# Kernel tuning notes

Measured on AMD Instinct MI355X. Metric: run time of the kernel, lower is better.

## Reference

```python
import jax, jax.numpy as jnp
import numpy as np

B, N, D, A = 2048, 32, 64, 8
MAX_ACTION = 1.0
VARIANCE = 1.0


def setup_inputs() -> dict:
    key = jax.random.key(0)
    k1, k2, k3, k4, k5 = jax.random.split(key, 5)
    mean = jax.random.normal(k1, (B, D), dtype=jnp.float32)
    # SPD covariance: small-scale L L^T + 0.1 I
    L = jax.random.normal(k2, (B, D, D), dtype=jnp.float32) * 0.05
    covariance = jnp.einsum('bij,bkj->bik', L, L) + 0.1 * jnp.eye(D, dtype=jnp.float32)
    centers = jax.random.normal(k3, (N, D), dtype=jnp.float32) * 0.5
    weights = jax.random.normal(k4, (N, A), dtype=jnp.float32) * 0.1
    lengthscales = jnp.ones((D,), dtype=jnp.float32) + 0.1 * jax.random.uniform(k5, (D,), dtype=jnp.float32)
    return {"mean": mean, "covariance": covariance, "centers": centers,
            "weights": weights, "lengthscales": lengthscales}


def squash_sin(mean, covariance, max_action):
    # mean: (B, K); covariance: (B, K, K)
    K = mean.shape[-1]
    ma = jnp.full((K,), max_action, dtype=mean.dtype)
    diag_cov = jnp.diagonal(covariance, axis1=-2, axis2=-1)          # (B, K)
    squashed_mean = ma * jnp.exp(-diag_cov / 2.0) * jnp.sin(mean)
    lq = -(diag_cov[..., :, None] + diag_cov[..., None, :]) / 2.0
    q = jnp.exp(lq)
    mean_diff = mean[..., :, None] - mean[..., None, :]
    mean_sum = mean[..., :, None] + mean[..., None, :]
    sq_cov = ((jnp.exp(lq + covariance) - q) * jnp.cos(mean_diff)
              - (jnp.exp(lq - covariance) - q) * jnp.cos(mean_sum))
    outer_max = ma[None, :] * ma[:, None]
    sq_cov = outer_max * sq_cov / 2.0
    # diag_embed of (B, K) -> (B, K, K)
    cross = (ma * jnp.exp(-diag_cov / 2.0) * jnp.cos(mean))[..., :, None] * jnp.eye(K, dtype=mean.dtype)
    return squashed_mean, sq_cov, cross


def reference(mean, covariance, centers, weights, lengthscales):
    b = mean.shape[0]
    inv_l = 1.0 / lengthscales                                        # (D,)
    # B_mat = diag(inv_l) @ cov @ diag(inv_l) + I  (B, D, D)
    B_mat = covariance * (inv_l[:, None] * inv_l[None, :]) + jnp.eye(D, dtype=mean.dtype)
    inp = centers[None, :, :] - mean[:, None, :]                      # (B, N, D)
    scaled_inp = inp * inv_l                                          # (B, N, D)
    t = jnp.swapaxes(jnp.linalg.solve(B_mat, jnp.swapaxes(scaled_inp, -1, -2)), -1, -2)  # (B, N, D)
    exp_term = jnp.exp(-0.5 * jnp.sum(scaled_inp * t, axis=-1))       # (B, N)
    _, log_det = jnp.linalg.slogdet(B_mat)                            # (B,)
    normalizer = VARIANCE * jnp.exp(-0.5 * log_det)
    phi_mean = normalizer[:, None] * exp_term                         # (B, N)
    action_mean = phi_mean @ weights                                  # (B, A)

    t_scaled = t * inv_l                                              # (B, N, D)
    cross_cov = jnp.einsum('bnd,bna->bda', t_scaled, phi_mean[..., None] * weights)  # (B, D, A)

    diff = centers[:, None, :] - centers[None, :, :]                  # (N, N, D)
    center_bar = (centers[:, None, :] + centers[None, :, :]) / 2.0    # (N, N, D)
    inv_lambda = 1.0 / lengthscales ** 2
    exp1 = -0.25 * jnp.sum(diff ** 2 * inv_lambda, axis=-1)           # (N, N)
    B_q = covariance + jnp.diag(lengthscales ** 2 / 2.0)[None]        # (B, D, D)
    z = center_bar[None] - mean[:, None, None, :]                     # (B, N, N, D)
    z_flat = z.reshape(b, N * N, D)
    solved = jnp.swapaxes(jnp.linalg.solve(B_q, jnp.swapaxes(z_flat, -1, -2)), -1, -2)
    exp2 = (-0.5 * jnp.sum(z_flat * solved, axis=-1)).reshape(b, N, N)
    log_det_lh = jnp.sum(jnp.log(lengthscales ** 2 / 2.0))
    _, log_det_bq = jnp.linalg.slogdet(B_q)
    c_q = jnp.exp(0.5 * (log_det_lh - log_det_bq))                    # (B,)
    Q = (VARIANCE ** 2) * c_q[:, None, None] * jnp.exp(exp1[None] + exp2)  # (B, N, N)

    action_cov = jnp.einsum('na,bnm,mc->bac', weights, Q, weights)    # (B, A, A)
    action_cov = action_cov - action_mean[:, :, None] * action_mean[:, None, :]
    action_cov = (action_cov + jnp.swapaxes(action_cov, -1, -2)) / 2.0
    action_cov = action_cov + jnp.eye(A, dtype=mean.dtype) * 1e-6

    action_mean, action_cov, C = squash_sin(action_mean, action_cov, MAX_ACTION)
    cross_cov = jnp.einsum('bda,bac->bdc', cross_cov, C)
    return (action_mean, action_cov, cross_cov)
```

## Files before the change

kernel.cpp:

```cpp
#include <hip/hip_runtime.h>
#include <math.h>


#define DD 64
#define NN 32
#define AA 8
#define NBATCH 2048
#define STR 68
#define W9 9

__device__ __forceinline__ float frl(float v, int lane) {
    return __int_as_float(__builtin_amdgcn_readlane(__float_as_int(v), lane));
}

__global__ void rbf_prep(const float* __restrict__ centers,
                         const float* __restrict__ ls,
                         float* __restrict__ ws) {
    __shared__ float cen_s[NN * DD];
    __shared__ float il2_s[DD];
    int t = threadIdx.x;
    for (int e = t; e < NN * DD; e += 256) cen_s[e] = centers[e];
    if (t < DD) { float l = ls[t]; il2_s[t] = 1.0f / (l * l); }
    __syncthreads();
    int p = blockIdx.x * 256 + t;
    if (p < NN * NN) {
        int n = p >> 5, m = p & 31;
        float acc = 0.f;
        for (int d = 0; d < DD; ++d) {
            float df = cen_s[n * DD + d] - cen_s[m * DD + d];
            acc += df * df * il2_s[d];
        }
        ws[p] = -0.25f * acc;
    }
    if (blockIdx.x == 0 && t < DD) {
        float l = ls[t];
        float v = logf(0.5f * l * l);
        #pragma unroll
        for (int o = 1; o < 64; o <<= 1) v += __shfl_xor(v, o, 64);
        if (t == 0) ws[NN * NN] = v;
    }
}

__device__ __forceinline__ void factor_panel(float (&A)[4][4], const int p,
    float* __restrict__ LmT, float* __restrict__ diag_s, float* __restrict__ invd_s,
    const int lw)
{
    const int rb  = lw & 15;
    const int cbl = lw >> 4;
    const int c0  = 16 * p + 4 * cbl;
    const int r0  = 4 * rb;
    #pragma unroll
    for (int jj = 0; jj < 16; ++jj) {
        const int q  = jj >> 2;
        const int ci = jj & 3;
        const int j  = 16 * p + jj;
        const int fsrc = rb | (q << 4);
        const int hsrc = (4 * p + cbl) | (q << 4);
        const int dsrc = (4 * p + q) | (q << 4);
        float d  = frl(A[ci][ci], dsrc);
        float f0 = __shfl(A[0][ci], fsrc, 64);
        float f1 = __shfl(A[1][ci], fsrc, 64);
        float f2 = __shfl(A[2][ci], fsrc, 64);
        float f3 = __shfl(A[3][ci], fsrc, 64);
        float h0 = __shfl(A[0][ci], hsrc, 64);
        float h1 = __shfl(A[1][ci], hsrc, 64);
        float h2 = __shfl(A[2][ci], hsrc, 64);
        float h3 = __shfl(A[3][ci], hsrc, 64);
        float id = __builtin_amdgcn_rcpf(d);
        float fr[4];
        fr[0] = (r0 + 0 > j) ? f0 : 0.f;
        fr[1] = (r0 + 1 > j) ? f1 : 0.f;
        fr[2] = (r0 + 2 > j) ? f2 : 0.f;
        fr[3] = (r0 + 3 > j) ? f3 : 0.f;
        float hc[4];
        hc[0] = (c0 + 0 > j) ? h0 * id : 0.f;
        hc[1] = (c0 + 1 > j) ? h1 * id : 0.f;
        hc[2] = (c0 + 2 > j) ? h2 * id : 0.f;
        hc[3] = (c0 + 3 > j) ? h3 * id : 0.f;
        #pragma unroll
        for (int s = 0; s < 4; ++s)
            #pragma unroll
            for (int c = 0; c < 4; ++c)
                A[s][c] -= fr[s] * hc[c];
        if (cbl == 0) {
            float4 v = make_float4(fr[0] * id, fr[1] * id, fr[2] * id, fr[3] * id);
            *(float4*)&LmT[j * STR + r0] = v;
        }
        if (lw == jj) { diag_s[j] = d; invd_s[j] = id; }
    }
}

__device__ __forceinline__ void trailing_one(float (&A)[4][4], const int p,
    const float* __restrict__ LmT, const float* __restrict__ diag_s,
    const int rb, const int cbX)
{
    #pragma unroll 2
    for (int kk = 0; kk < 16; ++kk) {
        const int k = 16 * p + kk;
        const float4 Lr = *(const float4*)&LmT[k * STR + 4 * rb];
        const float4 Lc = *(const float4*)&LmT[k * STR + 4 * cbX];
        const float dk = diag_s[k];
        const float h0 = Lc.x * dk, h1 = Lc.y * dk, h2 = Lc.z * dk, h3 = Lc.w * dk;
        A[0][0] -= Lr.x * h0; A[0][1] -= Lr.x * h1; A[0][2] -= Lr.x * h2; A[0][3] -= Lr.x * h3;
        A[1][0] -= Lr.y * h0; A[1][1] -= Lr.y * h1; A[1][2] -= Lr.y * h2; A[1][3] -= Lr.y * h3;
        A[2][0] -= Lr.z * h0; A[2][1] -= Lr.z * h1; A[2][2] -= Lr.z * h2; A[2][3] -= Lr.z * h3;
        A[3][0] -= Lr.w * h0; A[3][1] -= Lr.w * h1; A[3][2] -= Lr.w * h2; A[3][3] -= Lr.w * h3;
    }
}

__global__ __launch_bounds__(256, 3) void rbf_main(
    const float* __restrict__ mean,
    const float* __restrict__ cov,
    const float* __restrict__ centers,
    const float* __restrict__ weights,
    const float* __restrict__ ls,
    const float* __restrict__ ws,
    float* __restrict__ out)
{
    __shared__ __align__(16) float LmT1[DD * STR];
    __shared__ __align__(16) float U2s[DD * STR];
    __shared__ __align__(16) float phiwc[NN * AA];
    __shared__ float diag1[DD], invd1[DD], diag2[DD], invd2[DD];
    __shared__ float mean_s[DD], invl_s[DD], l2h_s[DD];
    __shared__ float w9_s[NN * W9], U_s[NN * W9];
    __shared__ float am_s[AA], acr_s[AA * W9], Ca_s[AA];
    __shared__ float ldlh_s;

    float* const LmT2 = U2s;
    float* const H_s  = U2s;
    float* const x_s  = U2s + NN * STR;
    float* const cp_s = U2s + NN * STR;

    const int t   = threadIdx.x;
    const int b   = blockIdx.x;
    const int lw  = t & 63;
    const int wv  = t >> 6;
    const int rb  = t & 15;
    const int cb  = t >> 4;
    const int cb1 = (cb + 8) & 15;
    const int wp1 = (wv + 2) & 3;
    const int l8  = t & 7;
    const float* cvb = cov + (size_t)b * DD * DD;

    if (t < DD) {
        float l = ls[t];
        invl_s[t] = 1.0f / l;
        l2h_s[t]  = 0.5f * l * l;
        mean_s[t] = mean[(size_t)b * DD + t];
    }
    w9_s[(t >> 3) * W9 + (t & 7)] = weights[t];
    if (t == 0) ldlh_s = ws[NN * NN];
    __syncthreads();

    float A1[4][4], A2[4][4];
    {
        #pragma unroll
        for (int c = 0; c < 4; ++c) {
            const int gr = 4 * cb + c;
            const float4 cv = *(const float4*)(cvb + (size_t)gr * DD + 4 * rb);
            A2[0][c] = cv.x + ((4*rb+0 == gr) ? l2h_s[gr] : 0.0f);
            A2[1][c] = cv.y + ((4*rb+1 == gr) ? l2h_s[gr] : 0.0f);
            A2[2][c] = cv.z + ((4*rb+2 == gr) ? l2h_s[gr] : 0.0f);
            A2[3][c] = cv.w + ((4*rb+3 == gr) ? l2h_s[gr] : 0.0f);
        }
        const float il0 = invl_s[4*rb+0], il1 = invl_s[4*rb+1],
                    il2 = invl_s[4*rb+2], il3 = invl_s[4*rb+3];
        #pragma unroll
        for (int c = 0; c < 4; ++c) {
            const int gr = 4 * cb1 + c;
            const float4 cv = *(const float4*)(cvb + (size_t)gr * DD + 4 * rb);
            const float ilc = invl_s[gr];
            A1[0][c] = cv.x * il0 * ilc + ((4*rb+0 == gr) ? 1.0f : 0.0f);
            A1[1][c] = cv.y * il1 * ilc + ((4*rb+1 == gr) ? 1.0f : 0.0f);
            A1[2][c] = cv.z * il2 * ilc + ((4*rb+2 == gr) ? 1.0f : 0.0f);
            A1[3][c] = cv.w * il3 * ilc + ((4*rb+3 == gr) ? 1.0f : 0.0f);
        }
    }

    if (wv == 0) factor_panel(A2, 0, LmT2, diag2, invd2, lw);
    if (wv == 2) factor_panel(A1, 0, LmT1, diag1, invd1, lw);
    #pragma unroll 1
    for (int p = 0; p < 3; ++p) {
        __syncthreads();
        if (wv  >= p + 1) trailing_one(A2, p, LmT2, diag2, rb, cb);
        if (wp1 >= p + 1) trailing_one(A1, p, LmT1, diag1, rb, cb1);
        if (wv == p + 1)         factor_panel(A2, p + 1, LmT2, diag2, invd2, lw);
        if (wv == ((p + 3) & 3)) factor_panel(A1, p + 1, LmT1, diag1, invd1, lw);
    }
    __syncthreads();

    float logdet1, cq;
    {
        float v1 = logf(diag1[lw]);
        float v2 = logf(diag2[lw]);
        #pragma unroll
        for (int o = 1; o < 64; o <<= 1) {
            v1 += __shfl_xor(v1, o, 64);
            v2 += __shfl_xor(v2, o, 64);
        }
        logdet1 = v1;
        cq = expf(0.5f * (ldlh_s - v2));
    }

    const int gr8 = lw >> 3;
    float xs0[8], xs1[8], xs2[8], xs3[8];
    if (wv == 0) {
        #pragma unroll
        for (int rr = 0; rr < 4; ++rr) {
            const int n = gr8 + 8 * rr;
            const float4 ca = *(const float4*)(centers + n * DD + 8 * l8);
            const float4 cz = *(const float4*)(centers + n * DD + 8 * l8 + 4);
            float da[8] = {ca.x,ca.y,ca.z,ca.w,cz.x,cz.y,cz.z,cz.w};
            float* xp = (rr == 0) ? xs0 : (rr == 1) ? xs1 : (rr == 2) ? xs2 : xs3;
            #pragma unroll
            for (int s = 0; s < 8; ++s) {
                const int i = 8 * l8 + s;
                xp[s] = (da[s] - mean_s[i]) * invl_s[i];
            }
        }
        for (int k8 = 0; k8 < 8; ++k8) {
            #pragma unroll
            for (int kk = 0; kk < 8; ++kk) {
                const int k = 8 * k8 + kk;
                const int src = (lw & 56) | k8;
                float z0 = __shfl(xs0[kk], src, 64);
                float z1 = __shfl(xs1[kk], src, 64);
                float z2 = __shfl(xs2[kk], src, 64);
                float z3 = __shfl(xs3[kk], src, 64);
                const float4 LA = *(const float4*)&LmT1[k * STR + 8 * l8];
                const float4 LB = *(const float4*)&LmT1[k * STR + 8 * l8 + 4];
                float l1[8] = {LA.x,LA.y,LA.z,LA.w,LB.x,LB.y,LB.z,LB.w};
                #pragma unroll
                for (int s = 0; s < 8; ++s) {
                    xs0[s] -= l1[s] * z0;
                    xs1[s] -= l1[s] * z1;
                    xs2[s] -= l1[s] * z2;
                    xs3[s] -= l1[s] * z3;
                }
            }
        }
        #pragma unroll
        for (int rr = 0; rr < 4; ++rr) {
            const int n = gr8 + 8 * rr;
            const float* xp = (rr == 0) ? xs0 : (rr == 1) ? xs1 : (rr == 2) ? xs2 : xs3;
            float qf = 0.f;
            #pragma unroll
            for (int s = 0; s < 8; ++s) qf += xp[s] * xp[s] * invd1[8 * l8 + s];
            qf += __shfl_xor(qf, 1, 64);
            qf += __shfl_xor(qf, 2, 64);
            qf += __shfl_xor(qf, 4, 64);
            float ph = expf(-0.5f * (logdet1 + qf));
            phiwc[n * AA + l8] = ph * w9_s[n * W9 + l8];
        }
    } else if (wv == 1) {
        float x0[8], x1v[8], x2v[8], x3v[8];
        #pragma unroll
        for (int rr = 0; rr < 4; ++rr) {
            const int n = gr8 + 8 * rr;
            const float4 ca = *(const float4*)(centers + n * DD + 8 * l8);
            const float4 cz = *(const float4*)(centers + n * DD + 8 * l8 + 4);
            float da[8] = {ca.x,ca.y,ca.z,ca.w,cz.x,cz.y,cz.z,cz.w};
            float* xp = (rr == 0) ? x0 : (rr == 1) ? x1v : (rr == 2) ? x2v : x3v;
            #pragma unroll
            for (int s = 0; s < 8; ++s) {
                const int i = 8 * l8 + s;
                xp[s] = 0.5f * (da[s] - mean_s[i]);
            }
        }
        for (int k8 = 0; k8 < 8; ++k8) {
            #pragma unroll
            for (int kk = 0; kk < 8; ++kk) {
                const int k = 8 * k8 + kk;
                const int src = (lw & 56) | k8;
                float z0 = __shfl(x0[kk],  src, 64);
                float z1 = __shfl(x1v[kk], src, 64);
                float z2 = __shfl(x2v[kk], src, 64);
                float z3 = __shfl(x3v[kk], src, 64);
                const float4 MA = *(const float4*)&LmT2[k * STR + 8 * l8];
                const float4 MB = *(const float4*)&LmT2[k * STR + 8 * l8 + 4];
                float l2[8] = {MA.x,MA.y,MA.z,MA.w,MB.x,MB.y,MB.z,MB.w};
                #pragma unroll
                for (int s = 0; s < 8; ++s) {
                    x0[s]  -= l2[s] * z0;
                    x1v[s] -= l2[s] * z1;
                    x2v[s] -= l2[s] * z2;
                    x3v[s] -= l2[s] * z3;
                }
            }
        }
        #pragma unroll
        for (int rr = 0; rr < 4; ++rr) {
            const int n = gr8 + 8 * rr;
            const float* xp = (rr == 0) ? x0 : (rr == 1) ? x1v : (rr == 2) ? x2v : x3v;
            float h[8];
            #pragma unroll
            for (int s = 0; s < 8; ++s) h[s] = xp[s] * sqrtf(invd2[8 * l8 + s]);
            *(float4*)&H_s[n * STR + 8 * l8]     = make_float4(h[0],h[1],h[2],h[3]);
            *(float4*)&H_s[n * STR + 8 * l8 + 4] = make_float4(h[4],h[5],h[6],h[7]);
        }
    }
    __syncthreads();

    if (wv == 0) {
        #pragma unroll
        for (int rr = 0; rr < 4; ++rr) {
            const int n = gr8 + 8 * rr;
            const float* xp = (rr == 0) ? xs0 : (rr == 1) ? xs1 : (rr == 2) ? xs2 : xs3;
            *(float4*)&x_s[n * STR + 8 * l8]     = make_float4(xp[0],xp[1],xp[2],xp[3]);
            *(float4*)&x_s[n * STR + 8 * l8 + 4] = make_float4(xp[4],xp[5],xp[6],xp[7]);
        }
        const int aa = lw >> 3;
        float y[8] = {0.f,0.f,0.f,0.f,0.f,0.f,0.f,0.f};
        for (int n = 0; n < NN; ++n) {
            const float pw = phiwc[n * AA + aa];
            const float4 xa = *(const float4*)&x_s[n * STR + 8 * l8];
            const float4 xb = *(const float4*)&x_s[n * STR + 8 * l8 + 4];
            y[0] += xa.x * pw; y[1] += xa.y * pw;
            y[2] += xa.z * pw; y[3] += xa.w * pw;
            y[4] += xb.x * pw; y[5] += xb.y * pw;
            y[6] += xb.z * pw; y[7] += xb.w * pw;
        }
        #pragma unroll
        for (int s = 0; s < 8; ++s) y[s] *= invd1[8 * l8 + s];
        for (int i8 = 7; i8 >= 0; --i8) {
            #pragma unroll
            for (int ii = 7; ii >= 0; --ii) {
                const int i = 8 * i8 + ii;
                const float4 r0 = *(const float4*)&LmT1[i * STR + 8 * l8];
                const float4 r1 = *(const float4*)&LmT1[i * STR + 8 * l8 + 4];
                float part = r0.x*y[0] + r0.y*y[1] + r0.z*y[2] + r0.w*y[3]
                           + r1.x*y[4] + r1.y*y[5] + r1.z*y[6] + r1.w*y[7];
                part += __shfl_xor(part, 1, 64);
                part += __shfl_xor(part, 2, 64);
                part += __shfl_xor(part, 4, 64);
                if (l8 == i8) y[ii] -= part;
            }
        }
        #pragma unroll
        for (int s = 0; s < 8; ++s)
            cp_s[(8 * l8 + s) * W9 + aa] = y[s] * invl_s[8 * l8 + s];
    } else if (wv == 3) {
        if (lw < AA) {
            const int a = lw;
            float am = 0.f;
            for (int n = 0; n < NN; ++n) am += phiwc[n * AA + a];
            am_s[a] = am;
        }
    } else {
        const int g16 = (lw >> 3) + 8 * (wv - 1);
        const int n0 = g16, n1 = g16 + 16;
        float acc0[4] = {0.f,0.f,0.f,0.f}, acc1[4] = {0.f,0.f,0.f,0.f};
        const int rot = 2 * l8;
        #pragma unroll 2
        for (int e = 0; e < 16; ++e) {
            const int e4 = 4 * ((e + rot) & 15);
            const float4 hn0 = *(const float4*)&H_s[n0 * STR + e4];
            const float4 hn1 = *(const float4*)&H_s[n1 * STR + e4];
            #pragma unroll
            for (int mm = 0; mm < 4; ++mm) {
                const float4 hm = *(const float4*)&H_s[(4 * l8 + mm) * STR + e4];
                {
                    float s0 = hn0.x + hm.x, s1 = hn0.y + hm.y;
                    float s2 = hn0.z + hm.z, s3 = hn0.w + hm.w;
                    acc0[mm] += s0*s0 + s1*s1 + s2*s2 + s3*s3;
                }
                {
                    float s0 = hn1.x + hm.x, s1 = hn1.y + hm.y;
                    float s2 = hn1.z + hm.z, s3 = hn1.w + hm.w;
                    acc1[mm] += s0*s0 + s1*s1 + s2*s2 + s3*s3;
                }
            }
        }
        const float4 e1a = *(const float4*)&ws[n0 * NN + 4 * l8];
        const float4 e1b = *(const float4*)&ws[n1 * NN + 4 * l8];
        float Q0a = cq * expf(e1a.x - 0.5f * acc0[0]);
        float Q1a = cq * expf(e1a.y - 0.5f * acc0[1]);
        float Q2a = cq * expf(e1a.z - 0.5f * acc0[2]);
        float Q3a = cq * expf(e1a.w - 0.5f * acc0[3]);
        float Q0b = cq * expf(e1b.x - 0.5f * acc1[0]);
        float Q1b = cq * expf(e1b.y - 0.5f * acc1[1]);
        float Q2b = cq * expf(e1b.z - 0.5f * acc1[2]);
        float Q3b = cq * expf(e1b.w - 0.5f * acc1[3]);
        float ua[8], ub[8];
        #pragma unroll
        for (int a = 0; a < 8; ++a) {
            const float w0 = w9_s[(4*l8+0)*W9 + a], w1 = w9_s[(4*l8+1)*W9 + a];
            const float w2 = w9_s[(4*l8+2)*W9 + a], w3 = w9_s[(4*l8+3)*W9 + a];
            ua[a] = Q0a*w0 + Q1a*w1 + Q2a*w2 + Q3a*w3;
            ub[a] = Q0b*w0 + Q1b*w1 + Q2b*w2 + Q3b*w3;
            ua[a] += __shfl_xor(ua[a], 1, 64);
            ua[a] += __shfl_xor(ua[a], 2, 64);
            ua[a] += __shfl_xor(ua[a], 4, 64);
            ub[a] += __shfl_xor(ub[a], 1, 64);
            ub[a] += __shfl_xor(ub[a], 2, 64);
            ub[a] += __shfl_xor(ub[a], 4, 64);
        }
        float uva = (l8 == 0) ? ua[0] : (l8 == 1) ? ua[1] : (l8 == 2) ? ua[2] : (l8 == 3) ? ua[3]
                  : (l8 == 4) ? ua[4] : (l8 == 5) ? ua[5] : (l8 == 6) ? ua[6] : ua[7];
        float uvb = (l8 == 0) ? ub[0] : (l8 == 1) ? ub[1] : (l8 == 2) ? ub[2] : (l8 == 3) ? ub[3]
                  : (l8 == 4) ? ub[4] : (l8 == 5) ? ub[5] : (l8 == 6) ? ub[6] : ub[7];
        U_s[n0 * W9 + l8] = uva;
        U_s[n1 * W9 + l8] = uvb;
    }
    __syncthreads();

    if (t < 64) {
        const int a = t >> 3, c = t & 7;
        float acc2 = 0.f;
        for (int n = 0; n < NN; ++n) acc2 += w9_s[n * W9 + a] * U_s[n * W9 + c];
        acr_s[a * W9 + c] = acc2;
    }
    __syncthreads();

    float* out0 = out;
    float* out1 = out + (size_t)NBATCH * AA;
    float* out2 = out + (size_t)NBATCH * AA + (size_t)NBATCH * AA * AA;
    if (t < 64) {
        const int a = t >> 3, c = t & 7;
        const float ama = am_s[a], amc = am_s[c];
        const float vac = 0.5f * (acr_s[a * W9 + c] + acr_s[c * W9 + a])
                        - ama * amc + ((a == c) ? 1e-6f : 0.0f);
        const float dca = acr_s[a * W9 + a] - ama * ama + 1e-6f;
        const float dcc = acr_s[c * W9 + c] - amc * amc + 1e-6f;
        const float q = expf(-0.5f * (dca + dcc));
        const float sq = 0.5f * q * (expm1f(vac) * cosf(ama - amc)
                                   - expm1f(-vac) * cosf(ama + amc));
        out1[(size_t)b * 64 + t] = sq;
        if (t < AA) {
            float dct = acr_s[t * W9 + t] - am_s[t] * am_s[t] + 1e-6f;
            float e = expf(-0.5f * dct);
            out0[(size_t)b * AA + t] = e * sinf(am_s[t]);
            Ca_s[t] = e * cosf(am_s[t]);
        }
    }
    __syncthreads();
    #pragma unroll
    for (int e = 0; e < 2; ++e) {
        int idx = t + 256 * e;
        out2[(size_t)b * 512 + idx] = cp_s[(idx >> 3) * W9 + (idx & 7)] * Ca_s[idx & 7];
    }
}

extern "C" void kernel_launch(void* const* d_in, const int* in_sizes, int n_in,
                              void* d_out, int out_size, void* d_ws, size_t ws_size,
                              hipStream_t stream) {
    (void)in_sizes; (void)n_in; (void)out_size; (void)ws_size;
    const float* mean    = (const float*)d_in[0];
    const float* cov     = (const float*)d_in[1];
    const float* centers = (const float*)d_in[2];
    const float* weights = (const float*)d_in[3];
    const float* ls      = (const float*)d_in[4];
    float* ws = (float*)d_ws;
    float* o  = (float*)d_out;
    rbf_prep<<<4, 256, 0, stream>>>(centers, ls, ws);
    rbf_main<<<NBATCH, 256, 0, stream>>>(mean, cov, centers, weights, ls, ws, o);
}
```

Before: 199.5 us.

## XOR-swizzle LmT shared layout and block the backward triangular solve

Stores the LDL factor rows in shared memory with an XOR swizzle over 8-wide column groups, and updates the Cholesky trailing loop and the forward solves to read through the same swizzle. This is meant to cut LDS bank conflicts. The backward substitution becomes a blocked 8x8 scheme: the diagonal block's values are broadcast by shuffle, solved redundantly in registers, and then the earlier blocks are updated. That replaces the three-step shuffle reduction per row. The swizzle has to stay consistent across every reader of LmT, or results will be wrong.

Measured after the change: 199.4 us. Within noise of the previous version (-0.0%).

```diff
diff --git a/kernel.cpp b/kernel.cpp
--- a/kernel.cpp
+++ b/kernel.cpp
@@ -83,8 +83,9 @@
             for (int c = 0; c < 4; ++c)
                 A[s][c] -= fr[s] * hc[c];
         if (cbl == 0) {
+            const int wo = 8 * ((rb >> 1) ^ ((j >> 3) & 7)) + 4 * (rb & 1);
             float4 v = make_float4(fr[0] * id, fr[1] * id, fr[2] * id, fr[3] * id);
-            *(float4*)&LmT[j * STR + r0] = v;
+            *(float4*)&LmT[j * STR + wo] = v;
         }
         if (lw == jj) { diag_s[j] = d; invd_s[j] = id; }
     }
@@ -97,8 +98,9 @@
     #pragma unroll 2
     for (int kk = 0; kk < 16; ++kk) {
         const int k = 16 * p + kk;
-        const float4 Lr = *(const float4*)&LmT[k * STR + 4 * rb];
-        const float4 Lc = *(const float4*)&LmT[k * STR + 4 * cbX];
+        const int cs = (k >> 3) & 7;
+        const float4 Lr = *(const float4*)&LmT[k * STR + 8*((rb >>1)^cs) + 4*(rb &1)];
+        const float4 Lc = *(const float4*)&LmT[k * STR + 8*((cbX>>1)^cs) + 4*(cbX&1)];
         const float dk = diag_s[k];
         const float h0 = Lc.x * dk, h1 = Lc.y * dk, h2 = Lc.z * dk, h3 = Lc.w * dk;
         A[0][0] -= Lr.x * h0; A[0][1] -= Lr.x * h1; A[0][2] -= Lr.x * h2; A[0][3] -= Lr.x * h3;
@@ -219,6 +221,7 @@
             }
         }
         for (int k8 = 0; k8 < 8; ++k8) {
+            const int kg = 8 * (l8 ^ k8);
             #pragma unroll
             for (int kk = 0; kk < 8; ++kk) {
                 const int k = 8 * k8 + kk;
@@ -227,8 +230,8 @@
                 float z1 = __shfl(xs1[kk], src, 64);
                 float z2 = __shfl(xs2[kk], src, 64);
                 float z3 = __shfl(xs3[kk], src, 64);
-                const float4 LA = *(const float4*)&LmT1[k * STR + 8 * l8];
-                const float4 LB = *(const float4*)&LmT1[k * STR + 8 * l8 + 4];
+                const float4 LA = *(const float4*)&LmT1[k * STR + kg];
+                const float4 LB = *(const float4*)&LmT1[k * STR + kg + 4];
                 float l1[8] = {LA.x,LA.y,LA.z,LA.w,LB.x,LB.y,LB.z,LB.w};
                 #pragma unroll
                 for (int s = 0; s < 8; ++s) {
@@ -268,6 +271,7 @@
             }
         }
         for (int k8 = 0; k8 < 8; ++k8) {
+            const int kg = 8 * (l8 ^ k8);
             #pragma unroll
             for (int kk = 0; kk < 8; ++kk) {
                 const int k = 8 * k8 + kk;
@@ -276,8 +280,8 @@
                 float z1 = __shfl(x1v[kk], src, 64);
                 float z2 = __shfl(x2v[kk], src, 64);
                 float z3 = __shfl(x3v[kk], src, 64);
-                const float4 MA = *(const float4*)&LmT2[k * STR + 8 * l8];
-                const float4 MB = *(const float4*)&LmT2[k * STR + 8 * l8 + 4];
+                const float4 MA = *(const float4*)&LmT2[k * STR + kg];
+                const float4 MB = *(const float4*)&LmT2[k * STR + kg + 4];
                 float l2[8] = {MA.x,MA.y,MA.z,MA.w,MB.x,MB.y,MB.z,MB.w};
                 #pragma unroll
                 for (int s = 0; s < 8; ++s) {
@@ -322,18 +326,32 @@
         }
         #pragma unroll
         for (int s = 0; s < 8; ++s) y[s] *= invd1[8 * l8 + s];
+        #pragma unroll 1
         for (int i8 = 7; i8 >= 0; --i8) {
+            const int srcl = (lw & 56) | i8;
+            float zs[8];
+            #pragma unroll
+            for (int s = 0; s < 8; ++s) zs[s] = __shfl(y[s], srcl, 64);
+            const float* rowb = &LmT1[(8 * i8) * STR];
             #pragma unroll
             for (int ii = 7; ii >= 0; --ii) {
-                const int i = 8 * i8 + ii;
-                const float4 r0 = *(const float4*)&LmT1[i * STR + 8 * l8];
-                const float4 r1 = *(const float4*)&LmT1[i * STR + 8 * l8 + 4];
-                float part = r0.x*y[0] + r0.y*y[1] + r0.z*y[2] + r0.w*y[3]
-                           + r1.x*y[4] + r1.y*y[5] + r1.z*y[6] + r1.w*y[7];
-                part += __shfl_xor(part, 1, 64);
-                part += __shfl_xor(part, 2, 64);
-                part += __shfl_xor(part, 4, 64);
-                if (l8 == i8) y[ii] -= part;
+                const float4 b0 = *(const float4*)&rowb[ii * STR + 0];
+                const float4 b1 = *(const float4*)&rowb[ii * STR + 4];
+                zs[ii] -= b0.x*zs[0] + b0.y*zs[1] + b0.z*zs[2] + b0.w*zs[3]
+                        + b1.x*zs[4] + b1.y*zs[5] + b1.z*zs[6] + b1.w*zs[7];
+            }
+            if (l8 == i8) {
+                #pragma unroll
+                for (int s = 0; s < 8; ++s) y[s] = zs[s];
+            } else if (l8 < i8) {
+                const int ug = 8 * (i8 ^ l8);
+                #pragma unroll
+                for (int s = 0; s < 8; ++s) {
+                    const float4 u0 = *(const float4*)&LmT1[(8*l8+s) * STR + ug];
+                    const float4 u1 = *(const float4*)&LmT1[(8*l8+s) * STR + ug + 4];
+                    y[s] -= u0.x*zs[0] + u0.y*zs[1] + u0.z*zs[2] + u0.w*zs[3]
+                          + u1.x*zs[4] + u1.y*zs[5] + u1.z*zs[6] + u1.w*zs[7];
+                }
             }
         }
         #pragma unroll
```
